# Kernel optimization log

Hardware: AMD Instinct MI355X
Metric: run time of the kernel (lower is better)

## Reference

```python
import jax, jax.numpy as jnp
import numpy as np

D_MODEL = 2048
D_INNER = 4096   # = d_ssm = nheads * headdim
NHEADS = 64      # = ngroups
DSTATE = 64      # = headdim (d_inner == ngroups * d_state)
D_XB = 1024      # GQA-style shared x/B width
XB_HEADS = D_XB // DSTATE    # 16
REP = NHEADS // XB_HEADS     # repeat_group = 4
DCONV = 4
CHUNK = 128
EPS = 1e-5
BATCH, SEQLEN = 1, 4096
D_IN_PROJ = 2 * D_INNER + 2 * D_XB + NHEADS  # d_mlp == 0
CONV_DIM = D_INNER + 2 * D_XB


def setup_inputs() -> dict:
    key = jax.random.key(0)
    ks = jax.random.split(key, 8)
    u = jax.random.normal(ks[0], (BATCH, SEQLEN, D_MODEL), jnp.float32)
    W_in = jax.random.normal(ks[1], (D_MODEL, D_IN_PROJ), jnp.float32) * np.float32(1.0 / np.sqrt(D_MODEL))
    conv_w = jax.random.uniform(ks[2], (CONV_DIM, DCONV), jnp.float32, -0.5, 0.5)
    conv_b = jnp.zeros((CONV_DIM,), jnp.float32)
    # dt_bias = inverse-softplus of dt sampled log-uniform in [dt_min, dt_max]
    dt = jnp.exp(jax.random.uniform(ks[3], (NHEADS,), jnp.float32) * np.float32(np.log(0.1) - np.log(0.001)) + np.float32(np.log(0.001)))
    dt = jnp.clip(dt, 1e-4, None)
    dt_bias = dt + jnp.log(-jnp.expm1(-dt))
    A_log = jnp.log(jax.random.uniform(ks[4], (NHEADS,), jnp.float32, 1.0, 16.0))
    D = jnp.ones((NHEADS,), jnp.float32)
    norm_weight = jnp.ones((D_INNER,), jnp.float32)
    W_out = jax.random.normal(ks[5], (D_INNER, D_MODEL), jnp.float32) * np.float32(1.0 / np.sqrt(D_INNER))
    return {"u": u, "W_in": W_in, "conv_w": conv_w, "conv_b": conv_b,
            "dt_bias": dt_bias, "A_log": A_log, "D": D,
            "norm_weight": norm_weight, "W_out": W_out}


def _ssd_chunked(x, dt, A, Bm, Cm):
    # x: (b,l,h,p), dt: (b,l,h) post-softplus, A: (h,) negative, Bm/Cm: (b,l,h,n)
    b, l, h, p = x.shape
    n = Bm.shape[-1]
    c, q = l // CHUNK, CHUNK
    rs = lambda t: t.reshape(b, c, q, *t.shape[2:])
    x_c, dt_c, B_c, C_c = rs(x), rs(dt), rs(Bm), rs(Cm)
    dA = dt_c * A                       # (b,c,q,h)
    cum = jnp.cumsum(dA, axis=2)        # (b,c,q,h)
    cumT = jnp.moveaxis(cum, 3, 2)      # (b,c,h,q)
    # intra-chunk: y_i += sum_{j<=i} (C_i.B_j) * exp(cum_i - cum_j) * dt_j * x_j
    diff = cumT[..., :, None] - cumT[..., None, :]               # (b,c,h,q,q)
    M = jnp.where(jnp.tril(jnp.ones((q, q), bool)), jnp.exp(diff), 0.0)
    xdt = x_c * dt_c[..., None]                                  # (b,c,q,h,p)
    G = jnp.einsum('bcihn,bcjhn->bchij', C_c, B_c)
    y = jnp.einsum('bchij,bcjhp->bcihp', G * M, xdt)
    # inter-chunk state passing
    decay_to_end = jnp.exp(cum[:, :, -1:, :] - cum)              # (b,c,q,h)
    S = jnp.einsum('bcjhn,bcjh,bcjhp->bchnp', B_c, decay_to_end, xdt)
    chunk_decay = jnp.exp(cum[:, :, -1, :])                      # (b,c,h)

    def step(H, inp):
        S_c, dec = inp
        return dec[..., None, None] * H + S_c, H

    H0 = jnp.zeros((b, h, n, p), x.dtype)
    _, Hprev = jax.lax.scan(step, H0, (jnp.moveaxis(S, 1, 0), jnp.moveaxis(chunk_decay, 1, 0)))
    Hprev = jnp.moveaxis(Hprev, 0, 1)                            # (b,c,h,n,p)
    y = y + jnp.einsum('bcihn,bcih,bchnp->bcihp', C_c, jnp.exp(cum), Hprev)
    return y.reshape(b, l, h, p)


def reference(u, W_in, conv_w, conv_b, dt_bias, A_log, D, norm_weight, W_out):
    b, l, _ = u.shape
    zxbcdt = u @ W_in                                            # (b,l,D_IN_PROJ)
    z = zxbcdt[..., :D_INNER]
    xBC = zxbcdt[..., D_INNER:D_INNER + CONV_DIM]
    dt = zxbcdt[..., D_INNER + CONV_DIM:]
    # depthwise causal conv1d + SiLU (padding d_conv-1 on the left, output len l)
    xp = jnp.pad(xBC, ((0, 0), (DCONV - 1, 0), (0, 0)))
    conv = conv_b + sum(xp[:, k:k + l, :] * conv_w[:, k] for k in range(DCONV))
    xBC = jax.nn.silu(conv)
    x = xBC[..., :D_XB]
    Bc = xBC[..., D_XB:2 * D_XB]
    Cc = xBC[..., 2 * D_XB:]
    # repeat_kv: (b,l,xb_heads,dstate) -> (b,l,nheads,dstate), interleaved repeats
    x = jnp.repeat(x.reshape(b, l, XB_HEADS, DSTATE), REP, axis=2)
    Bm = jnp.repeat(Bc.reshape(b, l, XB_HEADS, DSTATE), REP, axis=2)
    Cm = Cc.reshape(b, l, NHEADS, DSTATE)
    dt = jax.nn.softplus(dt + dt_bias)                           # dt_softplus=True
    A = -jnp.exp(A_log)
    y = _ssd_chunked(x, dt, A, Bm, Cm) + x * D[:, None]          # per-head D skip
    # gated RMSNorm: group size = d_ssm // ngroups = headdim, norm_before_gate=False
    yz = y * jax.nn.silu(z.reshape(b, l, NHEADS, DSTATE))
    normed = yz * jax.lax.rsqrt(jnp.mean(jnp.square(yz), axis=-1, keepdims=True) + EPS)
    out = normed.reshape(b, l, D_INNER) * norm_weight
    return out @ W_out
```

## Files before the change

kernel.cpp:

```cpp
#include <hip/hip_runtime.h>
#include <hip/hip_bf16.h>
#include <math.h>

typedef __hip_bfloat16 bf16;
typedef __attribute__((ext_vector_type(8))) short short8;
typedef __attribute__((ext_vector_type(4))) float f32x4;

#define D_MODEL   2048
#define D_INNER   4096
#define NHEADS    64
#define DSTATE    64
#define D_XB      1024
#define XB_HEADS  16
#define REP       4
#define DCONV     4
#define CHUNK     128
#define SEQLEN    4096
#define NCHUNK    (SEQLEN / CHUNK)
#define D_IN_PROJ (2*D_INNER + 2*D_XB + NHEADS)
#define NPAD      10368
#define CONV_DIM  (D_INNER + 2*D_XB)
#define EPS       1e-5f
#define LOG2E     1.44269504f

#define Z_BYTES    ((size_t)SEQLEN * D_INNER * 2)
#define RAW_BYTES  ((size_t)SEQLEN * CONV_DIM * 2)
#define DTP_BYTES  ((size_t)SEQLEN * NHEADS * 4)
#define CDEC_BYTES ((size_t)NCHUNK * NHEADS * 4)
#define CONV_BYTES ((size_t)SEQLEN * CONV_DIM * 2)
#define S_BYTES    ((size_t)NCHUNK * NHEADS * DSTATE * DSTATE * 4)
#define U_BYTES    ((size_t)SEQLEN * D_MODEL * 2)
#define RREG_BYTES (CONV_BYTES + S_BYTES)
#define WS_BYTES   (Z_BYTES + RAW_BYTES + DTP_BYTES + CDEC_BYTES + RREG_BYTES)

__device__ __forceinline__ short f2bf(float f) {
  bf16 h = __float2bfloat16(f);
  return *reinterpret_cast<short*>(&h);
}
__device__ __forceinline__ float bf2f(short s) {
  unsigned int u = ((unsigned int)(unsigned short)s) << 16;
  union { unsigned int u; float f; } c; c.u = u; return c.f;
}

__device__ __forceinline__ void gload_lds16(const void* g, void* l) {
  typedef __attribute__((address_space(1))) const unsigned int guint;
  typedef __attribute__((address_space(3))) unsigned int luint;
  __builtin_amdgcn_global_load_lds((guint*)g, (luint*)l, 16, 0, 0);
}

__device__ __forceinline__ char* swz128p(char* b, int r, int c) {
  int o = r * 128 + c * 2; o ^= (r & 7) << 4; return b + o;
}
__device__ __forceinline__ const char* swz128p(const char* b, int r, int c) {
  int o = r * 128 + c * 2; o ^= (r & 7) << 4; return b + o;
}
__device__ __forceinline__ char* swz256p(char* b, int r, int c) {
  int o = r * 256 + c * 2; o ^= (r & 15) << 4; return b + o;
}
__device__ __forceinline__ const char* swz256p(const char* b, int r, int c) {
  int o = r * 256 + c * 2; o ^= (r & 15) << 4; return b + o;
}

__global__ void fill_kernel(float* p, size_t n, float v) {
  size_t i = (size_t)blockIdx.x * blockDim.x + threadIdx.x;
  if (i < n) p[i] = v;
}

__global__ __launch_bounds__(256) void cast_f32_bf16(
    const float* __restrict__ in, short* __restrict__ out, size_t n4) {
  size_t i = (size_t)blockIdx.x * 256 + threadIdx.x;
  if (i >= n4) return;
  float4 v = ((const float4*)in)[i];
  short4 o;
  o.x = f2bf(v.x); o.y = f2bf(v.y); o.z = f2bf(v.z); o.w = f2bf(v.w);
  ((short4*)out)[i] = o;
}

__global__ __launch_bounds__(256) void transpose_cast(
    const float* __restrict__ in, short* __restrict__ out, int R, int C) {
  __shared__ float tile[32][33];
  const int c0 = blockIdx.x * 32;
  const int r0 = blockIdx.y * 32;
  const int tx = threadIdx.x & 31, ty = threadIdx.x >> 5;
#pragma unroll
  for (int i = 0; i < 4; ++i) {
    int r = ty + i * 8;
    float v = 0.f;
    if (c0 + tx < C) v = in[(size_t)(r0 + r) * C + c0 + tx];
    tile[r][tx] = v;
  }
  __syncthreads();
#pragma unroll
  for (int i = 0; i < 4; ++i) {
    int rr = ty + i * 8;
    out[(size_t)(c0 + rr) * R + r0 + tx] = f2bf(tile[tx][rr]);
  }
}

__device__ __forceinline__ void mfma_gemm_core(
    const short* __restrict__ A, const short* __restrict__ Bt, int K,
    int rowBase, int colBase, short As[128][64], short Bs[128][64],
    f32x4 acc[4][4]) {
  const int tid = threadIdx.x;
  const int lane = tid & 63;
  const int wid = tid >> 6;
  const int r_sub = lane >> 3;
  const int c8 = (lane & 7) * 8;
  const int wr = (wid >> 1) * 64;
  const int wc = (wid & 1) * 64;
  const int fr = lane & 15;
  const int kb = (lane >> 4) * 8;
  for (int k0 = 0; k0 < K; k0 += 64) {
#pragma unroll
    for (int i = 0; i < 4; ++i) {
      int c = i * 4 + wid;
      int r = c * 8 + r_sub;
      gload_lds16(A + (size_t)(rowBase + r) * K + k0 + c8, &As[r][c8]);
      gload_lds16(Bt + (size_t)(colBase + r) * K + k0 + c8, &Bs[r][c8]);
    }
    __syncthreads();
#pragma unroll
    for (int kk = 0; kk < 2; ++kk) {
      const int ko = kk * 32 + kb;
      short8 a[4], b[4];
#pragma unroll
      for (int m = 0; m < 4; ++m) a[m] = *(const short8*)&As[wr + m * 16 + fr][ko];
#pragma unroll
      for (int n = 0; n < 4; ++n) b[n] = *(const short8*)&Bs[wc + n * 16 + fr][ko];
#pragma unroll
      for (int m = 0; m < 4; ++m)
#pragma unroll
        for (int n = 0; n < 4; ++n)
          acc[m][n] = __builtin_amdgcn_mfma_f32_16x16x32_bf16(a[m], b[n], acc[m][n], 0, 0, 0);
    }
    __syncthreads();
  }
}

__global__ __launch_bounds__(256) void gemm1_mfma(
    const short* __restrict__ A, const short* __restrict__ Bt,
    bf16* __restrict__ z, bf16* __restrict__ raw, float* __restrict__ dtraw) {
  __shared__ short As[128][64];
  __shared__ short Bs[128][64];
  f32x4 acc[4][4] = {};
  const int bid = blockIdx.x;
  const int s = (bid & 7) * 324 + (bid >> 3);
  const int rowBase = (s & 31) * 128;
  const int colBase = (s >> 5) * 128;
  mfma_gemm_core(A, Bt, D_MODEL, rowBase, colBase, As, Bs, acc);
  const int lane = threadIdx.x & 63, wid = threadIdx.x >> 6;
  const int wr = (wid >> 1) * 64, wc = (wid & 1) * 64;
  const int r0 = rowBase + wr + (lane >> 4) * 4;
  const int cb = colBase + wc + (lane & 15);
#pragma unroll
  for (int m = 0; m < 4; ++m)
#pragma unroll
    for (int n = 0; n < 4; ++n) {
      int col = cb + n * 16;
#pragma unroll
      for (int j = 0; j < 4; ++j) {
        int row = r0 + m * 16 + j;
        float v = acc[m][n][j];
        if (col < D_INNER) {
          z[(size_t)row * D_INNER + col] = __float2bfloat16(v);
        } else if (col < D_INNER + CONV_DIM) {
          raw[(size_t)row * CONV_DIM + (col - D_INNER)] = __float2bfloat16(v);
        } else if (col < D_IN_PROJ) {
          dtraw[(size_t)row * NHEADS + (col - D_INNER - CONV_DIM)] = v;
        }
      }
    }
}

__global__ __launch_bounds__(256) void gemm2_mfma(
    const short* __restrict__ A, const short* __restrict__ Bt,
    float* __restrict__ C) {
  __shared__ short As[128][64];
  __shared__ short Bs[128][64];
  f32x4 acc[4][4] = {};
  const int bid = blockIdx.x;
  const int s = (bid & 7) * 64 + (bid >> 3);
  const int rowBase = (s & 31) * 128;
  const int colBase = (s >> 5) * 128;
  mfma_gemm_core(A, Bt, D_INNER, rowBase, colBase, As, Bs, acc);
  const int lane = threadIdx.x & 63, wid = threadIdx.x >> 6;
  const int wr = (wid >> 1) * 64, wc = (wid & 1) * 64;
  const int r0 = rowBase + wr + (lane >> 4) * 4;
  const int cb = colBase + wc + (lane & 15);
#pragma unroll
  for (int m = 0; m < 4; ++m)
#pragma unroll
    for (int n = 0; n < 4; ++n) {
      int col = cb + n * 16;
#pragma unroll
      for (int j = 0; j < 4; ++j)
        C[(size_t)(r0 + m * 16 + j) * D_MODEL + col] = acc[m][n][j];
    }
}

__global__ __launch_bounds__(256) void conv_silu_kernel(
    const bf16* __restrict__ raw, const float* __restrict__ cw,
    const float* __restrict__ cb, bf16* __restrict__ convout) {
  int idx = blockIdx.x * 256 + threadIdx.x;
  if (idx >= SEQLEN * (CONV_DIM / 8)) return;
  int t = idx / (CONV_DIM / 8);
  int c8 = (idx % (CONV_DIM / 8)) * 8;
  float acc[8];
  float4 w[8];
#pragma unroll
  for (int q = 0; q < 8; ++q) {
    acc[q] = cb[c8 + q];
    w[q] = ((const float4*)cw)[c8 + q];
  }
#pragma unroll
  for (int k = 0; k < DCONV; ++k) {
    int tt = t - (DCONV - 1) + k;
    if (tt < 0) continue;
    short8 v = *(const short8*)((const short*)raw + (size_t)tt * CONV_DIM + c8);
    const float* wk = (const float*)&w[0];
#pragma unroll
    for (int q = 0; q < 8; ++q)
      acc[q] += bf2f(v[q]) * ((const float*)&w[q])[k];
    (void)wk;
  }
  short8 o;
#pragma unroll
  for (int q = 0; q < 8; ++q) {
    float s = acc[q] / (1.f + expf(-acc[q]));
    o[q] = f2bf(s);
  }
  *(short8*)((short*)convout + (size_t)t * CONV_DIM + c8) = o;
}

__global__ __launch_bounds__(256) void dt_softplus_kernel(
    float* __restrict__ dtp, const float* __restrict__ dt_bias) {
  int idx = blockIdx.x * blockDim.x + threadIdx.x;
  if (idx >= SEQLEN * NHEADS) return;
  int h = idx & (NHEADS - 1);
  float x = dtp[idx] + dt_bias[h];
  dtp[idx] = (x > 20.f) ? x : log1pf(expf(x));
}

__global__ __launch_bounds__(256) void ssd_passA(
    const bf16* __restrict__ conv, const float* __restrict__ dtp,
    const float* __restrict__ A_log, short* __restrict__ Sbuf,
    float* __restrict__ cdec) {
  __shared__ __align__(16) char sBn[16384];
  __shared__ __align__(16) char sXn[16384];
  __shared__ __align__(16) char sBT[16384];
  __shared__ __align__(16) char sXT[16384];
  __shared__ float sdt[CHUNK], scum2[CHUNK], sw[CHUNK];
  const int chunk = blockIdx.x, h = blockIdx.y, g = h >> 2;
  const int tid = threadIdx.x, lane = tid & 63, wid = tid >> 6;
  const int t0 = chunk * CHUNK;
  const int fr = lane & 15, kq = lane >> 4;
  {
    const short* cg = (const short*)conv;
#pragma unroll
    for (int it = 0; it < 4; ++it) {
      int cid = tid + it * 256;
      int r = cid >> 3, c8 = (cid & 7) * 8;
      size_t rowoff = (size_t)(t0 + r) * CONV_DIM;
      *(short8*)swz128p(sBn, r, c8) = *(const short8*)(cg + rowoff + D_XB + g * 64 + c8);
      *(short8*)swz128p(sXn, r, c8) = *(const short8*)(cg + rowoff + g * 64 + c8);
    }
    if (tid < CHUNK) sdt[tid] = dtp[(size_t)(t0 + tid) * NHEADS + h];
  }
  __syncthreads();
  if (tid < CHUNK) {
    float Ah2 = -expf(A_log[h]) * LOG2E;
    float s_all = 0.f, s_le = 0.f;
    for (int i = 0; i < CHUNK; ++i) {
      float v = sdt[i] * Ah2;
      s_all += v;
      if (i <= tid) s_le += v;
    }
    scum2[tid] = s_le;
    sw[tid] = exp2f(s_all - s_le) * sdt[tid];
    if (tid == 0) cdec[chunk * NHEADS + h] = exp2f(s_all);
  }
  __syncthreads();
  {
    const int col = tid & 63, jb = (tid >> 6) * 32;
#pragma unroll
    for (int it = 0; it < 32; ++it) {
      int j = jb + it;
      *(short*)swz256p(sBT, col, j) = *(const short*)swz128p(sBn, j, col);
      float xv = bf2f(*(const short*)swz128p(sXn, j, col));
      *(short*)swz256p(sXT, col, j) = f2bf(xv * sw[j]);
    }
  }
  __syncthreads();
  f32x4 acc[4] = {};
#pragma unroll
  for (int ks = 0; ks < 4; ++ks) {
    short8 a = *(const short8*)swz256p(sXT, wid * 16 + fr, ks * 32 + kq * 8);
    short8 b[4];
#pragma unroll
    for (int n = 0; n < 4; ++n) b[n] = *(const short8*)swz256p(sBT, n * 16 + fr, ks * 32 + kq * 8);
#pragma unroll
    for (int n = 0; n < 4; ++n)
      acc[n] = __builtin_amdgcn_mfma_f32_16x16x32_bf16(a, b[n], acc[n], 0, 0, 0);
  }
  short* So = Sbuf + ((size_t)(chunk * NHEADS + h)) * (DSTATE * DSTATE);
#pragma unroll
  for (int n = 0; n < 4; ++n)
#pragma unroll
    for (int jj = 0; jj < 4; ++jj) {
      int p = wid * 16 + kq * 4 + jj;
      int nc = n * 16 + fr;
      So[p * 64 + nc] = f2bf(acc[n][jj]);
    }
}

__global__ __launch_bounds__(256) void ssd_passB(
    short* __restrict__ Sbuf, const float* __restrict__ cdec) {
  const int h = blockIdx.x;
  const int base = blockIdx.y * 1024 + threadIdx.x * 4;
  float H[4] = {};
  for (int c = 0; c < NCHUNK; ++c) {
    short4* Sc = (short4*)(Sbuf + ((size_t)(c * NHEADS + h)) * (DSTATE * DSTATE) + base);
    short4 v = *Sc;
    short4 o;
    o.x = f2bf(H[0]); o.y = f2bf(H[1]); o.z = f2bf(H[2]); o.w = f2bf(H[3]);
    *Sc = o;
    float dec = cdec[c * NHEADS + h];
    H[0] = dec * H[0] + bf2f(v.x);
    H[1] = dec * H[1] + bf2f(v.y);
    H[2] = dec * H[2] + bf2f(v.z);
    H[3] = dec * H[3] + bf2f(v.w);
  }
}

__global__ __launch_bounds__(256) void ssd_passC(
    const bf16* __restrict__ z, const bf16* __restrict__ conv,
    const float* __restrict__ dtp, const float* __restrict__ A_log,
    const float* __restrict__ Dv, const float* __restrict__ nw,
    const short* __restrict__ Hprev, bf16* __restrict__ normed) {
  __shared__ __align__(16) char sC[16384];
  __shared__ __align__(16) char sBX[16384];
  __shared__ __align__(16) char sP[32768];
  __shared__ __align__(16) char sST[8192];
  __shared__ float sdt[CHUNK], scum2[CHUNK];
  const int chunk = blockIdx.x, h = blockIdx.y, g = h >> 2;
  const int tid = threadIdx.x, lane = tid & 63, wid = tid >> 6;
  const int t0 = chunk * CHUNK;
  const int fr = lane & 15, kq = lane >> 4;
  const int wi = wid * 32;
  {
    const short* cg = (const short*)conv;
#pragma unroll
    for (int it = 0; it < 4; ++it) {
      int cid = tid + it * 256;
      int r = cid >> 3, c8 = (cid & 7) * 8;
      size_t rowoff = (size_t)(t0 + r) * CONV_DIM;
      *(short8*)swz128p(sC, r, c8) = *(const short8*)(cg + rowoff + 2 * D_XB + h * 64 + c8);
      *(short8*)swz128p(sBX, r, c8) = *(const short8*)(cg + rowoff + D_XB + g * 64 + c8);
      *(short8*)swz128p(sP + 16384, r, c8) = *(const short8*)(cg + rowoff + g * 64 + c8);
    }
    if (tid < CHUNK) sdt[tid] = dtp[(size_t)(t0 + tid) * NHEADS + h];
  }
  __syncthreads();
  if (tid < CHUNK) {
    float Ah2 = -expf(A_log[h]) * LOG2E;
    float s_le = 0.f;
    for (int i = 0; i <= tid; ++i) s_le += sdt[i] * Ah2;
    scum2[tid] = s_le;
  }
  __syncthreads();
  f32x4 accG[2][8] = {};
#pragma unroll
  for (int ks = 0; ks < 2; ++ks) {
    short8 a[2], b[8];
#pragma unroll
    for (int m = 0; m < 2; ++m)
      a[m] = *(const short8*)swz128p(sC, wi + m * 16 + fr, ks * 32 + kq * 8);
#pragma unroll
    for (int n = 0; n < 8; ++n)
      b[n] = *(const short8*)swz128p(sBX, n * 16 + fr, ks * 32 + kq * 8);
#pragma unroll
    for (int m = 0; m < 2; ++m)
#pragma unroll
      for (int n = 0; n < 8; ++n)
        accG[m][n] = __builtin_amdgcn_mfma_f32_16x16x32_bf16(a[m], b[n], accG[m][n], 0, 0, 0);
  }
  __syncthreads();
  {
    const int p = tid & 63, jb = (tid >> 6) * 32;
#pragma unroll
    for (int it = 0; it < 32; ++it) {
      int j = jb + it;
      *(short*)swz256p(sBX, p, j) = *(const short*)swz128p(sP + 16384, j, p);
    }
    const short* Hp = Hprev + ((size_t)(chunk * NHEADS + h)) * (DSTATE * DSTATE);
#pragma unroll
    for (int it = 0; it < 2; ++it) {
      int cid = tid + it * 256;
      int pr = cid >> 3, c8 = (cid & 7) * 8;
      *(short8*)swz128p(sST, pr, c8) = *(const short8*)(Hp + pr * 64 + c8);
    }
  }
  __syncthreads();
#pragma unroll
  for (int m = 0; m < 2; ++m)
#pragma unroll
    for (int jj = 0; jj < 4; ++jj) {
      int i = wi + m * 16 + kq * 4 + jj;
      float ci = scum2[i];
#pragma unroll
      for (int n = 0; n < 8; ++n) {
        int j = n * 16 + fr;
        float w = (j <= i) ? exp2f(ci - scum2[j]) * sdt[j] : 0.f;
        *(short*)swz256p(sP, i, j) = f2bf(accG[m][n][jj] * w);
      }
    }
  __syncthreads();
  f32x4 acc1[2][4] = {};
#pragma unroll
  for (int ks = 0; ks < 4; ++ks) {
    short8 a[2], b[4];
#pragma unroll
    for (int m = 0; m < 2; ++m)
      a[m] = *(const short8*)swz256p(sP, wi + m * 16 + fr, ks * 32 + kq * 8);
#pragma unroll
    for (int n = 0; n < 4; ++n)
      b[n] = *(const short8*)swz256p(sBX, n * 16 + fr, ks * 32 + kq * 8);
#pragma unroll
    for (int m = 0; m < 2; ++m)
#pragma unroll
      for (int n = 0; n < 4; ++n)
        acc1[m][n] = __builtin_amdgcn_mfma_f32_16x16x32_bf16(a[m], b[n], acc1[m][n], 0, 0, 0);
  }
  f32x4 acc2[2][4] = {};
#pragma unroll
  for (int ks = 0; ks < 2; ++ks) {
    short8 a[2], b[4];
#pragma unroll
    for (int m = 0; m < 2; ++m)
      a[m] = *(const short8*)swz128p(sC, wi + m * 16 + fr, ks * 32 + kq * 8);
#pragma unroll
    for (int n = 0; n < 4; ++n)
      b[n] = *(const short8*)swz128p(sST, n * 16 + fr, ks * 32 + kq * 8);
#pragma unroll
    for (int m = 0; m < 2; ++m)
#pragma unroll
      for (int n = 0; n < 4; ++n)
        acc2[m][n] = __builtin_amdgcn_mfma_f32_16x16x32_bf16(a[m], b[n], acc2[m][n], 0, 0, 0);
  }
  const float Dh = Dv[h];
#pragma unroll
  for (int m = 0; m < 2; ++m)
#pragma unroll
    for (int jj = 0; jj < 4; ++jj) {
      int i = wi + m * 16 + kq * 4 + jj;
      int t = t0 + i;
      float e2 = exp2f(scum2[i]);
      float vs[4];
      float ss = 0.f;
#pragma unroll
      for (int n = 0; n < 4; ++n) {
        int p = n * 16 + fr;
        float xv = bf2f(((const short*)conv)[(size_t)t * CONV_DIM + g * 64 + p]);
        float zv = bf2f(((const short*)z)[(size_t)t * D_INNER + h * 64 + p]);
        float y = acc1[m][n][jj] + e2 * acc2[m][n][jj] + xv * Dh;
        float sz = zv / (1.f + expf(-zv));
        float v = y * sz;
        vs[n] = v;
        ss += v * v;
      }
      ss += __shfl_xor(ss, 1);
      ss += __shfl_xor(ss, 2);
      ss += __shfl_xor(ss, 4);
      ss += __shfl_xor(ss, 8);
      float rinv = rsqrtf(ss * (1.f / 64.f) + EPS);
#pragma unroll
      for (int n = 0; n < 4; ++n) {
        int p = n * 16 + fr;
        ((short*)normed)[(size_t)t * D_INNER + h * 64 + p] = f2bf(vs[n] * rinv * nw[h * 64 + p]);
      }
    }
}

extern "C" void kernel_launch(void* const* d_in, const int* in_sizes, int n_in,
                              void* d_out, int out_size, void* d_ws, size_t ws_size,
                              hipStream_t stream) {
  const float* u       = (const float*)d_in[0];
  const float* W_in    = (const float*)d_in[1];
  const float* conv_w  = (const float*)d_in[2];
  const float* conv_b  = (const float*)d_in[3];
  const float* dt_bias = (const float*)d_in[4];
  const float* A_log   = (const float*)d_in[5];
  const float* Dv      = (const float*)d_in[6];
  const float* norm_w  = (const float*)d_in[7];
  const float* W_out   = (const float*)d_in[8];
  float* out = (float*)d_out;

  if (ws_size < WS_BYTES) {
    size_t n = (size_t)out_size;
    fill_kernel<<<(n + 255) / 256, 256, 0, stream>>>(out, n, 1000.0f);
    return;
  }

  char* wsb   = (char*)d_ws;
  bf16*  z    = (bf16*)(wsb);
  bf16*  raw  = (bf16*)(wsb + Z_BYTES);
  float* dtp  = (float*)(wsb + Z_BYTES + RAW_BYTES);
  float* cdec = (float*)(wsb + Z_BYTES + RAW_BYTES + DTP_BYTES);
  char*  R    = wsb + Z_BYTES + RAW_BYTES + DTP_BYTES + CDEC_BYTES;
  short* u_bf  = (short*)(R);
  short* WinT  = (short*)(R + U_BYTES);
  bf16*  conv  = (bf16*)(R);
  short* Sbuf  = (short*)(R + CONV_BYTES);
  short* WoutT = (short*)(R);
  bf16*  normed = raw;

  cast_f32_bf16<<<(U_BYTES / 8 + 255) / 256, 256, 0, stream>>>(u, u_bf, U_BYTES / 8);
  {
    dim3 grid(NPAD / 32, D_MODEL / 32);
    transpose_cast<<<grid, 256, 0, stream>>>(W_in, WinT, D_MODEL, D_IN_PROJ);
  }
  gemm1_mfma<<<(NPAD / 128) * (SEQLEN / 128), 256, 0, stream>>>(u_bf, WinT, z, raw, dtp);
  conv_silu_kernel<<<(SEQLEN * (CONV_DIM / 8) + 255) / 256, 256, 0, stream>>>(raw, conv_w, conv_b, conv);
  dt_softplus_kernel<<<(SEQLEN * NHEADS + 255) / 256, 256, 0, stream>>>(dtp, dt_bias);
  {
    dim3 grid(NCHUNK, NHEADS);
    ssd_passA<<<grid, 256, 0, stream>>>(conv, dtp, A_log, Sbuf, cdec);
  }
  {
    dim3 grid(NHEADS, 4);
    ssd_passB<<<grid, 256, 0, stream>>>(Sbuf, cdec);
  }
  {
    dim3 grid(NCHUNK, NHEADS);
    ssd_passC<<<grid, 256, 0, stream>>>(z, conv, dtp, A_log, Dv, norm_w, Sbuf, normed);
  }
  {
    dim3 grid(D_MODEL / 32, D_INNER / 32);
    transpose_cast<<<grid, 256, 0, stream>>>(W_out, WoutT, D_INNER, D_MODEL);
  }
  gemm2_mfma<<<(D_MODEL / 128) * (SEQLEN / 128), 256, 0, stream>>>((const short*)normed, WoutT, out);
}
```

Baseline: 664.9 us.

## Replace GEMMs with 256x256-tile double-buffered swizzled-LDS MFMA kernels

```diff
diff --git a/kernel.cpp b/kernel.cpp
--- a/kernel.cpp
+++ b/kernel.cpp
@@ -18,7 +18,7 @@
 #define SEQLEN    4096
 #define NCHUNK    (SEQLEN / CHUNK)
 #define D_IN_PROJ (2*D_INNER + 2*D_XB + NHEADS)
-#define NPAD      10368
+#define NPAD      10496
 #define CONV_DIM  (D_INNER + 2*D_XB)
 #define EPS       1e-5f
 #define LOG2E     1.44269504f
@@ -30,6 +30,7 @@
 #define CONV_BYTES ((size_t)SEQLEN * CONV_DIM * 2)
 #define S_BYTES    ((size_t)NCHUNK * NHEADS * DSTATE * DSTATE * 4)
 #define U_BYTES    ((size_t)SEQLEN * D_MODEL * 2)
+#define WINT_BYTES ((size_t)NPAD * D_MODEL * 2)
 #define RREG_BYTES (CONV_BYTES + S_BYTES)
 #define WS_BYTES   (Z_BYTES + RAW_BYTES + DTP_BYTES + CDEC_BYTES + RREG_BYTES)
 
@@ -97,70 +98,102 @@
   }
 }
 
-__device__ __forceinline__ void mfma_gemm_core(
-    const short* __restrict__ A, const short* __restrict__ Bt, int K,
-    int rowBase, int colBase, short As[128][64], short Bs[128][64],
-    f32x4 acc[4][4]) {
-  const int tid = threadIdx.x;
-  const int lane = tid & 63;
-  const int wid = tid >> 6;
-  const int r_sub = lane >> 3;
-  const int c8 = (lane & 7) * 8;
-  const int wr = (wid >> 1) * 64;
-  const int wc = (wid & 1) * 64;
-  const int fr = lane & 15;
-  const int kb = (lane >> 4) * 8;
-  for (int k0 = 0; k0 < K; k0 += 64) {
-#pragma unroll
-    for (int i = 0; i < 4; ++i) {
-      int c = i * 4 + wid;
-      int r = c * 8 + r_sub;
-      gload_lds16(A + (size_t)(rowBase + r) * K + k0 + c8, &As[r][c8]);
-      gload_lds16(Bt + (size_t)(colBase + r) * K + k0 + c8, &Bs[r][c8]);
-    }
-    __syncthreads();
-#pragma unroll
-    for (int kk = 0; kk < 2; ++kk) {
-      const int ko = kk * 32 + kb;
-      short8 a[4], b[4];
-#pragma unroll
-      for (int m = 0; m < 4; ++m) a[m] = *(const short8*)&As[wr + m * 16 + fr][ko];
-#pragma unroll
-      for (int n = 0; n < 4; ++n) b[n] = *(const short8*)&Bs[wc + n * 16 + fr][ko];
-#pragma unroll
-      for (int m = 0; m < 4; ++m)
-#pragma unroll
-        for (int n = 0; n < 4; ++n)
-          acc[m][n] = __builtin_amdgcn_mfma_f32_16x16x32_bf16(a[m], b[n], acc[m][n], 0, 0, 0);
-    }
-    __syncthreads();
-  }
-}
-
-__global__ __launch_bounds__(256) void gemm1_mfma(
+
+__device__ __forceinline__ void stage_half(const char* gtile, int rowbytes,
+                                           char* ldst, int tid) {
+#pragma unroll
+  for (int i = 0; i < 2; ++i) {
+    int cid = i * 512 + tid;
+    int r = cid >> 2;
+    int pos = ((cid & 3) * 16) ^ (((r >> 1) & 3) << 4);
+    gload_lds16(gtile + (size_t)r * rowbytes + pos, ldst + cid * 16);
+  }
+}
+
+__device__ __forceinline__ void compute_phase(const char* ldsA, const char* ldsB,
+    int kh16, int wm, int wn, int mh, int fr, int kqb, f32x4 (&acc)[8][4]) {
+  short8 a[4], b[4];
+#pragma unroll
+  for (int m = 0; m < 4; ++m) {
+    int r = wm * 128 + mh * 64 + m * 16 + fr;
+    a[m] = *(const short8*)(ldsA + kh16 + r * 64 + (kqb ^ (((r >> 1) & 3) << 4)));
+  }
+#pragma unroll
+  for (int n = 0; n < 4; ++n) {
+    int r = wn * 64 + n * 16 + fr;
+    b[n] = *(const short8*)(ldsB + kh16 + r * 64 + (kqb ^ (((r >> 1) & 3) << 4)));
+  }
+  __builtin_amdgcn_s_setprio(1);
+#pragma unroll
+  for (int m = 0; m < 4; ++m)
+#pragma unroll
+    for (int n = 0; n < 4; ++n)
+      acc[mh * 4 + m][n] = __builtin_amdgcn_mfma_f32_16x16x32_bf16(a[m], b[n], acc[mh * 4 + m][n], 0, 0, 0);
+  __builtin_amdgcn_s_setprio(0);
+}
+
+#define WAIT_BAR(N)                                        \
+  asm volatile("s_waitcnt vmcnt(" #N ")" ::: "memory");    \
+  __builtin_amdgcn_s_barrier();                            \
+  __builtin_amdgcn_sched_barrier(0);
+
+__device__ __forceinline__ void gemm256_core(const short* A, const short* Bt, int K,
+    int rowBase, int colBase, char* lds, f32x4 (&acc)[8][4]) {
+  const int tid = threadIdx.x, lane = tid & 63;
+  const int w = tid >> 6, wm = w >> 2, wn = w & 3;
+  const int fr = lane & 15, kqb = (lane >> 4) * 16;
+  const int NT = K >> 6;
+  const int rb = K * 2;
+  char* ldsA = lds;
+  char* ldsB = lds + 65536;
+  const char* Ag = (const char*)(A + (size_t)rowBase * K);
+  const char* Bg = (const char*)(Bt + (size_t)colBase * K);
+  stage_half(Ag, rb, ldsA, tid);
+  stage_half(Bg, rb, ldsB, tid);
+  stage_half(Ag + 64, rb, ldsA + 16384, tid);
+  stage_half(Bg + 64, rb, ldsB + 16384, tid);
+  WAIT_BAR(4)
+  for (int t = 0; t < NT; ++t) {
+    const int cb = (t & 1) * 32768, nb = ((t + 1) & 1) * 32768;
+    const size_t ko = (size_t)(t + 1) * 128;
+    const bool more = (t + 1 < NT);
+    if (more) stage_half(Ag + ko, rb, ldsA + nb, tid);
+    compute_phase(ldsA + cb, ldsB + cb, 0, wm, wn, 0, fr, kqb, acc);
+    if (more) stage_half(Bg + ko, rb, ldsB + nb, tid);
+    compute_phase(ldsA + cb, ldsB + cb, 0, wm, wn, 1, fr, kqb, acc);
+    if (more) { WAIT_BAR(4) } else { WAIT_BAR(0) }
+    if (more) stage_half(Ag + ko + 64, rb, ldsA + nb + 16384, tid);
+    compute_phase(ldsA + cb, ldsB + cb, 16384, wm, wn, 0, fr, kqb, acc);
+    if (more) stage_half(Bg + ko + 64, rb, ldsB + nb + 16384, tid);
+    compute_phase(ldsA + cb, ldsB + cb, 16384, wm, wn, 1, fr, kqb, acc);
+    if (more) { WAIT_BAR(4) } else { WAIT_BAR(0) }
+  }
+}
+
+__global__ __launch_bounds__(512) void gemm1_8ph(
     const short* __restrict__ A, const short* __restrict__ Bt,
     bf16* __restrict__ z, bf16* __restrict__ raw, float* __restrict__ dtraw) {
-  __shared__ short As[128][64];
-  __shared__ short Bs[128][64];
-  f32x4 acc[4][4] = {};
+  __shared__ __align__(16) char lds[131072];
+  f32x4 acc[8][4] = {};
   const int bid = blockIdx.x;
-  const int s = (bid & 7) * 324 + (bid >> 3);
-  const int rowBase = (s & 31) * 128;
-  const int colBase = (s >> 5) * 128;
-  mfma_gemm_core(A, Bt, D_MODEL, rowBase, colBase, As, Bs, acc);
-  const int lane = threadIdx.x & 63, wid = threadIdx.x >> 6;
-  const int wr = (wid >> 1) * 64, wc = (wid & 1) * 64;
-  const int r0 = rowBase + wr + (lane >> 4) * 4;
-  const int cb = colBase + wc + (lane & 15);
-#pragma unroll
-  for (int m = 0; m < 4; ++m)
+  const int s = (bid & 7) * 82 + (bid >> 3);
+  const int rowBase = (s & 15) * 256;
+  const int colBase = (s >> 4) * 256;
+  gemm256_core(A, Bt, D_MODEL, rowBase, colBase, lds, acc);
+  const int lane = threadIdx.x & 63, w = threadIdx.x >> 6;
+  const int wm = w >> 2, wn = w & 3;
+  const int fr = lane & 15, kq = lane >> 4;
+  const int r0 = rowBase + wm * 128 + kq * 4;
+  const int c0 = colBase + wn * 64 + fr;
+#pragma unroll
+  for (int M = 0; M < 8; ++M)
 #pragma unroll
     for (int n = 0; n < 4; ++n) {
-      int col = cb + n * 16;
+      int col = c0 + n * 16;
 #pragma unroll
       for (int j = 0; j < 4; ++j) {
-        int row = r0 + m * 16 + j;
-        float v = acc[m][n][j];
+        int row = r0 + M * 16 + j;
+        float v = acc[M][n][j];
         if (col < D_INNER) {
           z[(size_t)row * D_INNER + col] = __float2bfloat16(v);
         } else if (col < D_INNER + CONV_DIM) {
@@ -172,29 +205,29 @@
     }
 }
 
-__global__ __launch_bounds__(256) void gemm2_mfma(
+__global__ __launch_bounds__(512) void gemm2_8ph(
     const short* __restrict__ A, const short* __restrict__ Bt,
     float* __restrict__ C) {
-  __shared__ short As[128][64];
-  __shared__ short Bs[128][64];
-  f32x4 acc[4][4] = {};
+  __shared__ __align__(16) char lds[131072];
+  f32x4 acc[8][4] = {};
   const int bid = blockIdx.x;
-  const int s = (bid & 7) * 64 + (bid >> 3);
-  const int rowBase = (s & 31) * 128;
-  const int colBase = (s >> 5) * 128;
-  mfma_gemm_core(A, Bt, D_INNER, rowBase, colBase, As, Bs, acc);
-  const int lane = threadIdx.x & 63, wid = threadIdx.x >> 6;
-  const int wr = (wid >> 1) * 64, wc = (wid & 1) * 64;
-  const int r0 = rowBase + wr + (lane >> 4) * 4;
-  const int cb = colBase + wc + (lane & 15);
-#pragma unroll
-  for (int m = 0; m < 4; ++m)
+  const int s = (bid & 7) * 16 + (bid >> 3);
+  const int rowBase = (s & 15) * 256;
+  const int colBase = (s >> 4) * 256;
+  gemm256_core(A, Bt, D_INNER, rowBase, colBase, lds, acc);
+  const int lane = threadIdx.x & 63, w = threadIdx.x >> 6;
+  const int wm = w >> 2, wn = w & 3;
+  const int fr = lane & 15, kq = lane >> 4;
+  const int r0 = rowBase + wm * 128 + kq * 4;
+  const int c0 = colBase + wn * 64 + fr;
+#pragma unroll
+  for (int M = 0; M < 8; ++M)
 #pragma unroll
     for (int n = 0; n < 4; ++n) {
-      int col = cb + n * 16;
+      int col = c0 + n * 16;
 #pragma unroll
       for (int j = 0; j < 4; ++j)
-        C[(size_t)(r0 + m * 16 + j) * D_MODEL + col] = acc[m][n][j];
+        C[(size_t)(r0 + M * 16 + j) * D_MODEL + col] = acc[M][n][j];
     }
 }
 
@@ -217,11 +250,9 @@
     int tt = t - (DCONV - 1) + k;
     if (tt < 0) continue;
     short8 v = *(const short8*)((const short*)raw + (size_t)tt * CONV_DIM + c8);
-    const float* wk = (const float*)&w[0];
 #pragma unroll
     for (int q = 0; q < 8; ++q)
       acc[q] += bf2f(v[q]) * ((const float*)&w[q])[k];
-    (void)wk;
   }
   short8 o;
 #pragma unroll
@@ -519,7 +550,7 @@
     dim3 grid(NPAD / 32, D_MODEL / 32);
     transpose_cast<<<grid, 256, 0, stream>>>(W_in, WinT, D_MODEL, D_IN_PROJ);
   }
-  gemm1_mfma<<<(NPAD / 128) * (SEQLEN / 128), 256, 0, stream>>>(u_bf, WinT, z, raw, dtp);
+  gemm1_8ph<<<(NPAD / 256) * (SEQLEN / 256), 512, 0, stream>>>(u_bf, WinT, z, raw, dtp);
   conv_silu_kernel<<<(SEQLEN * (CONV_DIM / 8) + 255) / 256, 256, 0, stream>>>(raw, conv_w, conv_b, conv);
   dt_softplus_kernel<<<(SEQLEN * NHEADS + 255) / 256, 256, 0, stream>>>(dtp, dt_bias);
   {
@@ -538,5 +569,5 @@
     dim3 grid(D_MODEL / 32, D_INNER / 32);
     transpose_cast<<<grid, 256, 0, stream>>>(W_out, WoutT, D_INNER, D_MODEL);
   }
-  gemm2_mfma<<<(D_MODEL / 128) * (SEQLEN / 128), 256, 0, stream>>>((const short*)normed, WoutT, out);
-}
+  gemm2_8ph<<<(D_MODEL / 256) * (SEQLEN / 256), 512, 0, stream>>>((const short*)normed, WoutT, out);
+}
```

Result: faster. 579.9 us (-12.8%).
